# Optimization experiments

Measured on AMD Instinct MI355X. Metric: run time of the kernel, lower is better.

## Reference

```python
import jax, jax.numpy as jnp
import numpy as np

N, EM, EW, L, S = 20000, 100000, 25000, 128, 6


def _mlp(x, W1, b1, W2, b2, g, beta):
    # Linear -> ReLU -> Linear -> LayerNorm
    h = jax.nn.relu(x @ W1 + b1) @ W2 + b2
    mu = jnp.mean(h, axis=-1, keepdims=True)
    var = jnp.mean((h - mu) ** 2, axis=-1, keepdims=True)
    return g * (h - mu) * jax.lax.rsqrt(var + 1e-5) + beta


def _scatter_mean(attr, recv, n):
    s = jax.ops.segment_sum(attr, recv, num_segments=n)
    c = jax.ops.segment_sum(jnp.ones((attr.shape[0], 1), attr.dtype), recv, num_segments=n)
    return s / jnp.maximum(c, 1.0)


def setup_inputs() -> dict:
    key = jax.random.key(0)
    ks = jax.random.split(key, 16)

    def w(k, shape, fan_in):
        return (jax.random.normal(k, shape, jnp.float32) / np.sqrt(fan_in).astype(np.float32))

    inp = {
        'x': jax.random.normal(ks[0], (N, L), jnp.float32),
        'mesh_edge_attr': jax.random.normal(ks[1], (EM, L), jnp.float32),
        'world_edge_attr': jax.random.normal(ks[2], (EW, L), jnp.float32),
        'mesh_edge_index': jax.random.randint(ks[3], (2, EM), 0, N),
        'world_edge_index': jax.random.randint(ks[4], (2, EW), 0, N),
    }
    i = 5
    for pre in ('me', 'we', 'nd'):
        inp[pre + '_W1'] = w(ks[i], (S, 3 * L, L), 3 * L); i += 1
        inp[pre + '_b1'] = jnp.zeros((S, L), jnp.float32)
        inp[pre + '_W2'] = w(ks[i], (S, L, L), L); i += 1
        inp[pre + '_b2'] = jnp.zeros((S, L), jnp.float32)
        inp[pre + '_g'] = jnp.ones((S, L), jnp.float32)
        inp[pre + '_beta'] = jnp.zeros((S, L), jnp.float32)
    return inp


def reference(x, mesh_edge_attr, world_edge_attr, mesh_edge_index, world_edge_index,
              me_W1, me_b1, me_W2, me_b2, me_g, me_beta,
              we_W1, we_b1, we_W2, we_b2, we_g, we_beta,
              nd_W1, nd_b1, nd_W2, nd_b2, nd_g, nd_beta):
    ms, mr = mesh_edge_index[0], mesh_edge_index[1]
    ws, wr = world_edge_index[0], world_edge_index[1]
    n = x.shape[0]

    def step(carry, p):
        x, mea, wea = carry
        (mW1, mb1, mW2, mb2, mg, mbe,
         wW1, wb1, wW2, wb2, wg, wbe,
         nW1, nb1, nW2, nb2, ng, nbe) = p
        # EdgeModel: gather + concat + MLP, residual into edge attrs
        mea = mea + _mlp(jnp.concatenate([x[ms], x[mr], mea], axis=-1), mW1, mb1, mW2, mb2, mg, mbe)
        wea = wea + _mlp(jnp.concatenate([x[ws], x[wr], wea], axis=-1), wW1, wb1, wW2, wb2, wg, wbe)
        # NodeModel: scatter-mean over both edge sets + concat + MLP, residual
        agg = jnp.concatenate([x, _scatter_mean(mea, mr, n), _scatter_mean(wea, wr, n)], axis=-1)
        x = x + _mlp(agg, nW1, nb1, nW2, nb2, ng, nbe)
        return (x, mea, wea), None

    params = (me_W1, me_b1, me_W2, me_b2, me_g, me_beta,
              we_W1, we_b1, we_W2, we_b2, we_g, we_beta,
              nd_W1, nd_b1, nd_W2, nd_b2, nd_g, nd_beta)
    (x, mea, wea), _ = jax.lax.scan(step, (x, mesh_edge_attr, world_edge_attr), params)
    return x, mea, wea
```

## Files before the change

### kernel.cpp

```cpp
#include <hip/hip_runtime.h>

constexpr int LDIM  = 128;
constexpr int NNODE = 20000;
constexpr int EM_N  = 100000;
constexpr int EW_N  = 25000;
constexpr int NSTEP = 6;

typedef short bf16x8 __attribute__((ext_vector_type(8)));
typedef short bf16x4 __attribute__((ext_vector_type(4)));
typedef float f32x4  __attribute__((ext_vector_type(4)));

struct MlpParams {
  const float* x;
  const float* attrIn;
  float*       attrOut;
  const int*   src;
  const int*   dst;
  float*       sum1;
  float*       sum2;
  const float* inv1;
  const float* inv2;
  const short* W1H;
  const short* W2H;
  const float* b1;
  const float* b2;
  const float* gam;
  const float* bet;
  int nRows;
};

__device__ __forceinline__ short f2b(float f) {
  unsigned int u = __float_as_uint(f);
  u = (u + 0x7fffu + ((u >> 16) & 1u)) >> 16;
  return (short)u;
}
__device__ __forceinline__ float b2f(short s) {
  return __uint_as_float(((unsigned int)(unsigned short)s) << 16);
}
__device__ __forceinline__ bf16x4 cvt4(float4 a, float sc) {
  bf16x4 o;
  o[0] = f2b(a.x * sc); o[1] = f2b(a.y * sc);
  o[2] = f2b(a.z * sc); o[3] = f2b(a.w * sc);
  return o;
}

template<bool IS_EDGE>
__launch_bounds__(256, 3)
__global__ void mlp_kernel(MlpParams pmA, MlpParams pmB, int blocksA) {
  const bool isA = (int)blockIdx.x < blocksA;
  const MlpParams P = isA ? pmA : pmB;
  const int bid  = isA ? (int)blockIdx.x : (int)blockIdx.x - blocksA;
  const int row0 = bid * 128;

  __shared__ __align__(16) short Hbuf[128][136];
  __shared__ __align__(16) short Bhi[128][40];
  __shared__ float b1s[128], b2s[128], gs[128], bes[128];
  __shared__ int   idxa[128], idxb[128];
  __shared__ float inv1s[128], inv2s[128];
  __shared__ float sumL[2][128], sqL[2][128];
  __shared__ float muL[128], rsL[128];

  short (*Abuf)[40] = (short (*)[40])(&Hbuf[0][0]);

  const int t = threadIdx.x;

  if (t < 128) {
    b1s[t] = P.b1[t];
    gs[t]  = P.gam[t];
    if (IS_EDGE) {
      int r = row0 + t;
      idxa[t] = (r < P.nRows) ? P.src[r] : 0;
    } else {
      int r = min(row0 + t, P.nRows - 1);
      inv1s[t] = P.inv1[r];
    }
  } else {
    int t2 = t - 128;
    b2s[t2] = P.b2[t2];
    bes[t2] = P.bet[t2];
    if (IS_EDGE) {
      int r = row0 + t2;
      idxb[t2] = (r < P.nRows) ? P.dst[r] : 0;
    } else {
      int r = min(row0 + t2, P.nRows - 1);
      inv2s[t2] = P.inv2[r];
    }
  }
  __syncthreads();

  const int l   = t & 63;
  const int wid = t >> 6;
  const int wr  = wid >> 1, wcc = wid & 1;
  const int lr  = l & 15,  lg  = l >> 4;

  const int  srow  = t >> 1, sh = t & 1;
  const int  sgRow = row0 + srow;
  const bool sval  = sgRow < P.nRows;
  const int  sgC   = sval ? sgRow : 0;
  const float vmask = sval ? 1.f : 0.f;

  const float* base0; const float* base1; const float* base2;
  float sc1v = vmask, sc2v = vmask;
  if (IS_EDGE) {
    base0 = P.x + (size_t)idxa[srow] * LDIM + sh * 16;
    base1 = P.x + (size_t)idxb[srow] * LDIM + sh * 16;
    base2 = P.attrIn + (size_t)sgC * LDIM + sh * 16;
  } else {
    base0 = P.x    + (size_t)sgC * LDIM + sh * 16;
    base1 = P.sum1 + (size_t)sgC * LDIM + sh * 16;
    base2 = P.sum2 + (size_t)sgC * LDIM + sh * 16;
    sc1v = inv1s[srow] * vmask;
    sc2v = inv2s[srow] * vmask;
  }

  const int wrow = t >> 1, wsh = t & 1;
  const short* w1base = P.W1H + (size_t)wrow * 384 + wsh * 16;

  f32x4 acc[4][4];
#pragma unroll
  for (int i = 0; i < 4; ++i)
#pragma unroll
    for (int j = 0; j < 4; ++j) acc[i][j] = f32x4{0.f, 0.f, 0.f, 0.f};

  float4 pA0, pA1, pA2, pA3;
  bf16x8 pW0, pW1;
  {
    const float4* bp = (const float4*)base0;
    pA0 = bp[0]; pA1 = bp[1]; pA2 = bp[2]; pA3 = bp[3];
    pW0 = *(const bf16x8*)w1base;
    pW1 = *(const bf16x8*)(w1base + 8);
  }

#pragma unroll
  for (int kc = 0; kc < 12; ++kc) {
    const int seg = kc >> 2, part = kc & 3;
    if (kc > 0) __syncthreads();
    {
      const float scK = (seg == 0) ? vmask : (seg == 1) ? sc1v : sc2v;
      *(bf16x4*)&Abuf[srow][sh * 16 + 0]  = cvt4(pA0, scK);
      *(bf16x4*)&Abuf[srow][sh * 16 + 4]  = cvt4(pA1, scK);
      *(bf16x4*)&Abuf[srow][sh * 16 + 8]  = cvt4(pA2, scK);
      *(bf16x4*)&Abuf[srow][sh * 16 + 12] = cvt4(pA3, scK);
      *(bf16x8*)&Bhi[wrow][wsh * 16]     = pW0;
      *(bf16x8*)&Bhi[wrow][wsh * 16 + 8] = pW1;
      if constexpr (!IS_EDGE) {
        if (seg != 0 && sval) {
          float4 z = {0.f, 0.f, 0.f, 0.f};
          float4* zp = (float4*)((seg == 1 ? base1 : base2) + part * 32);
          zp[0] = z; zp[1] = z; zp[2] = z; zp[3] = z;
        }
      }
    }
    __syncthreads();
    if (kc < 11) {
      const int kn = kc + 1, segn = kn >> 2, partn = kn & 3;
      const float4* bp = (const float4*)((segn == 0 ? base0 : segn == 1 ? base1 : base2) + partn * 32);
      pA0 = bp[0]; pA1 = bp[1]; pA2 = bp[2]; pA3 = bp[3];
      pW0 = *(const bf16x8*)(w1base + kn * 32);
      pW1 = *(const bf16x8*)(w1base + kn * 32 + 8);
    }
    bf16x8 av[4], bh[4];
#pragma unroll
    for (int mi = 0; mi < 4; ++mi)
      av[mi] = *(const bf16x8*)&Abuf[wr * 64 + mi * 16 + lr][lg * 8];
#pragma unroll
    for (int ni = 0; ni < 4; ++ni)
      bh[ni] = *(const bf16x8*)&Bhi[wcc * 64 + ni * 16 + lr][lg * 8];
#pragma unroll
    for (int mi = 0; mi < 4; ++mi)
#pragma unroll
      for (int ni = 0; ni < 4; ++ni)
        acc[mi][ni] = __builtin_amdgcn_mfma_f32_16x16x32_bf16(av[mi], bh[ni], acc[mi][ni], 0, 0, 0);
  }

  __syncthreads();

#pragma unroll
  for (int rt = 0; rt < 4; ++rt)
#pragma unroll
    for (int ct = 0; ct < 4; ++ct) {
      const int cc = wcc * 64 + ct * 16 + lr;
      const float bb = b1s[cc];
#pragma unroll
      for (int q = 0; q < 4; ++q) {
        const int rr = wr * 64 + rt * 16 + lg * 4 + q;
        Hbuf[rr][cc] = f2b(fmaxf(acc[rt][ct][q] + bb, 0.f));
      }
    }

  f32x4 acc2[4][4];
#pragma unroll
  for (int i = 0; i < 4; ++i)
#pragma unroll
    for (int j = 0; j < 4; ++j) acc2[i][j] = f32x4{0.f, 0.f, 0.f, 0.f};

  const short* w2base = P.W2H + (size_t)wrow * 128 + wsh * 16;
  bf16x8 q0 = *(const bf16x8*)w2base;
  bf16x8 q1 = *(const bf16x8*)(w2base + 8);

#pragma unroll
  for (int kc = 0; kc < 4; ++kc) {
    __syncthreads();
    {
      *(bf16x8*)&Bhi[wrow][wsh * 16]     = q0;
      *(bf16x8*)&Bhi[wrow][wsh * 16 + 8] = q1;
    }
    __syncthreads();
    if (kc < 3) {
      q0 = *(const bf16x8*)(w2base + (kc + 1) * 32);
      q1 = *(const bf16x8*)(w2base + (kc + 1) * 32 + 8);
    }
    bf16x8 av2[4], bh2[4];
#pragma unroll
    for (int rt = 0; rt < 4; ++rt)
      av2[rt] = *(const bf16x8*)&Hbuf[wr * 64 + rt * 16 + lr][kc * 32 + lg * 8];
#pragma unroll
    for (int ct = 0; ct < 4; ++ct)
      bh2[ct] = *(const bf16x8*)&Bhi[wcc * 64 + ct * 16 + lr][lg * 8];
#pragma unroll
    for (int rt = 0; rt < 4; ++rt)
#pragma unroll
      for (int ct = 0; ct < 4; ++ct)
        acc2[rt][ct] = __builtin_amdgcn_mfma_f32_16x16x32_bf16(av2[rt], bh2[ct], acc2[rt][ct], 0, 0, 0);
  }

  float s1[4][4], s2[4][4];
#pragma unroll
  for (int rt = 0; rt < 4; ++rt)
#pragma unroll
    for (int q = 0; q < 4; ++q) { s1[rt][q] = 0.f; s2[rt][q] = 0.f; }
#pragma unroll
  for (int rt = 0; rt < 4; ++rt)
#pragma unroll
    for (int ct = 0; ct < 4; ++ct) {
      const float bb = b2s[wcc * 64 + ct * 16 + lr];
#pragma unroll
      for (int q = 0; q < 4; ++q) {
        float v = acc2[rt][ct][q] + bb;
        acc2[rt][ct][q] = v;
        s1[rt][q] += v;
        s2[rt][q] += v * v;
      }
    }
#pragma unroll
  for (int m = 1; m < 16; m <<= 1) {
#pragma unroll
    for (int rt = 0; rt < 4; ++rt)
#pragma unroll
      for (int q = 0; q < 4; ++q) {
        s1[rt][q] += __shfl_xor(s1[rt][q], m);
        s2[rt][q] += __shfl_xor(s2[rt][q], m);
      }
  }
  __syncthreads();
  {
    const int rt = lr >> 2, q = lr & 3;
    const int rr = wr * 64 + rt * 16 + lg * 4 + q;
    sumL[wcc][rr] = s1[rt][q];
    sqL[wcc][rr]  = s2[rt][q];
  }
  __syncthreads();
  if (t < 128) {
    const float tot = sumL[0][t] + sumL[1][t];
    const float tsq = sqL[0][t] + sqL[1][t];
    const float mu  = tot * (1.0f / 128.0f);
    const float var = tsq * (1.0f / 128.0f) - mu * mu;
    muL[t] = mu;
    rsL[t] = rsqrtf(var + 1e-5f);
  }
  __syncthreads();

#pragma unroll
  for (int rt = 0; rt < 4; ++rt) {
#pragma unroll
    for (int q = 0; q < 4; ++q) {
      const int rr = wr * 64 + rt * 16 + lg * 4 + q;
      const int grow = row0 + rr;
      if (grow < P.nRows) {
        const float mu = muL[rr], rs = rsL[rr];
        const float* rin = P.attrIn + (size_t)grow * LDIM;
        float* rout = P.attrOut + (size_t)grow * LDIM;
        float* ssum = nullptr;
        if (IS_EDGE) ssum = P.sum1 + (size_t)idxb[rr] * LDIM;
#pragma unroll
        for (int ct = 0; ct < 4; ++ct) {
          const int cc = wcc * 64 + ct * 16 + lr;
          const float o = gs[cc] * (acc2[rt][ct][q] - mu) * rs + bes[cc] + rin[cc];
          rout[cc] = o;
          if (IS_EDGE) atomicAdd(ssum + cc, o);
        }
      }
    }
  }
}

__global__ void prep_weights(const float* w1a, const float* w1b, const float* w1c,
                             const float* w2a, const float* w2b, const float* w2c,
                             short* w1h, short* w2h) {
  int i = blockIdx.x * 256 + threadIdx.x;
  constexpr int N1 = 18 * 128 * 384;
  constexpr int N2 = 18 * 128 * 128;
  if (i < N1) {
    int g = i / (128 * 384);
    int rem = i - g * (128 * 384);
    int n = rem / 384, k = rem - n * 384;
    int m = g / 6, s = g - m * 6;
    const float* src = (m == 0) ? w1a : (m == 1) ? w1b : w1c;
    w1h[i] = f2b(src[(size_t)s * (384 * 128) + (size_t)k * 128 + n]);
  } else if (i < N1 + N2) {
    int j = i - N1;
    int g = j / (128 * 128);
    int rem = j - g * (128 * 128);
    int n = rem / 128, k = rem - n * 128;
    int m = g / 6, s = g - m * 6;
    const float* src = (m == 0) ? w2a : (m == 1) ? w2b : w2c;
    w2h[j] = f2b(src[(size_t)s * (128 * 128) + (size_t)k * 128 + n]);
  }
}

__global__ void prep_deg(const int* mr, const int* wrcv, int* degm, int* degw) {
  int i = blockIdx.x * 256 + threadIdx.x;
  if (i < EM_N) atomicAdd(&degm[mr[i]], 1);
  else if (i < EM_N + EW_N) atomicAdd(&degw[wrcv[i - EM_N]], 1);
}

__global__ void prep_inv(const int* degm, const int* degw, float* invm, float* invw) {
  int i = blockIdx.x * 256 + threadIdx.x;
  if (i < NNODE) {
    invm[i] = 1.0f / fmaxf((float)degm[i], 1.0f);
    invw[i] = 1.0f / fmaxf((float)degw[i], 1.0f);
  }
}

extern "C" void kernel_launch(void* const* d_in, const int* in_sizes, int n_in,
                              void* d_out, int out_size, void* d_ws, size_t ws_size,
                              hipStream_t stream) {
  (void)in_sizes; (void)n_in; (void)out_size; (void)ws_size;
  const float* x_in   = (const float*)d_in[0];
  const float* mea_in = (const float*)d_in[1];
  const float* wea_in = (const float*)d_in[2];
  const int*   mei    = (const int*)d_in[3];
  const int*   wei    = (const int*)d_in[4];
  const float* W1s[3] = { (const float*)d_in[5],  (const float*)d_in[11], (const float*)d_in[17] };
  const float* B1s[3] = { (const float*)d_in[6],  (const float*)d_in[12], (const float*)d_in[18] };
  const float* W2s[3] = { (const float*)d_in[7],  (const float*)d_in[13], (const float*)d_in[19] };
  const float* B2s[3] = { (const float*)d_in[8],  (const float*)d_in[14], (const float*)d_in[20] };
  const float* Gs[3]  = { (const float*)d_in[9],  (const float*)d_in[15], (const float*)d_in[21] };
  const float* Be[3]  = { (const float*)d_in[10], (const float*)d_in[16], (const float*)d_in[22] };

  float* xo  = (float*)d_out;
  float* meo = xo  + (size_t)NNODE * LDIM;
  float* weo = meo + (size_t)EM_N * LDIM;

  float* msum = (float*)d_ws;
  float* wsum = msum + (size_t)NNODE * LDIM;
  int*   degm = (int*)(wsum + (size_t)NNODE * LDIM);
  int*   degw = degm + NNODE;
  float* invm = (float*)(degw + NNODE);
  float* invw = invm + NNODE;
  short* w1h  = (short*)(invw + NNODE);
  short* w2h  = w1h + (size_t)18 * 128 * 384;

  size_t zbytes = (size_t)2 * NNODE * LDIM * 4 + (size_t)2 * NNODE * 4;
  hipMemsetAsync(d_ws, 0, zbytes, stream);

  {
    int tot = 18 * 128 * 384 + 18 * 128 * 128;
    prep_weights<<<dim3((tot + 255) / 256), 256, 0, stream>>>(
        W1s[0], W1s[1], W1s[2], W2s[0], W2s[1], W2s[2], w1h, w2h);
  }
  prep_deg<<<dim3((EM_N + EW_N + 255) / 256), 256, 0, stream>>>(mei + EM_N, wei + EW_N, degm, degw);
  prep_inv<<<dim3((NNODE + 255) / 256), 256, 0, stream>>>(degm, degw, invm, invw);

  const int MB = (EM_N + 127) / 128;
  const int WB = (EW_N + 127) / 128;
  const int NB = (NNODE + 127) / 128;

  const float* xc = x_in;
  const float* mc = mea_in;
  const float* wc = wea_in;

  for (int s = 0; s < NSTEP; ++s) {
    MlpParams pm{}, pw{}, pn{};

    pm.x = xc; pm.attrIn = mc; pm.attrOut = meo;
    pm.src = mei; pm.dst = mei + EM_N;
    pm.sum1 = msum;
    pm.W1H = w1h + (size_t)(0 * 6 + s) * 128 * 384;
    pm.W2H = w2h + (size_t)(0 * 6 + s) * 128 * 128;
    pm.b1 = B1s[0] + s * LDIM; pm.b2 = B2s[0] + s * LDIM;
    pm.gam = Gs[0] + s * LDIM; pm.bet = Be[0] + s * LDIM;
    pm.nRows = EM_N;

    pw.x = xc; pw.attrIn = wc; pw.attrOut = weo;
    pw.src = wei; pw.dst = wei + EW_N;
    pw.sum1 = wsum;
    pw.W1H = w1h + (size_t)(1 * 6 + s) * 128 * 384;
    pw.W2H = w2h + (size_t)(1 * 6 + s) * 128 * 128;
    pw.b1 = B1s[1] + s * LDIM; pw.b2 = B2s[1] + s * LDIM;
    pw.gam = Gs[1] + s * LDIM; pw.bet = Be[1] + s * LDIM;
    pw.nRows = EW_N;

    mlp_kernel<true><<<dim3(MB + WB), 256, 0, stream>>>(pm, pw, MB);

    pn.x = xc; pn.attrIn = xc; pn.attrOut = xo;
    pn.sum1 = msum; pn.sum2 = wsum; pn.inv1 = invm; pn.inv2 = invw;
    pn.W1H = w1h + (size_t)(2 * 6 + s) * 128 * 384;
    pn.W2H = w2h + (size_t)(2 * 6 + s) * 128 * 128;
    pn.b1 = B1s[2] + s * LDIM; pn.b2 = B2s[2] + s * LDIM;
    pn.gam = Gs[2] + s * LDIM; pn.bet = Be[2] + s * LDIM;
    pn.nRows = NNODE;

    mlp_kernel<false><<<dim3(NB), 256, 0, stream>>>(pn, pn, NB);

    xc = xo; mc = meo; wc = weo;
  }
}
```

Measured before the change: 919.6 us.

## Double-buffer LDS staging in MLP GEMMs with single barrier per chunk

Converts both GEMM k-loops in the fused MLP kernel to double-buffered LDS staging, with two A buffers carved from Hbuf and two weight buffers. Global loads run two chunks ahead in register sets, and each iteration needs one barrier instead of two, using a custom waitcnt+s_barrier helper. This is meant to cut barrier stalls and overlap global loads with MFMA. In exchange it uses more registers and LDS, so launch bounds drop from 3 to 2 blocks per SM, which lowers occupancy.

New measurement: 1.047 ms. 1.14x slower.

```diff
diff --git a/kernel.cpp b/kernel.cpp
--- a/kernel.cpp
+++ b/kernel.cpp
@@ -44,8 +44,14 @@
   return o;
 }
 
+__device__ __forceinline__ void barrier_lds() {
+  asm volatile("s_waitcnt lgkmcnt(0)" ::: "memory");
+  __builtin_amdgcn_sched_barrier(0);
+  __builtin_amdgcn_s_barrier();
+}
+
 template<bool IS_EDGE>
-__launch_bounds__(256, 3)
+__launch_bounds__(256, 2)
 __global__ void mlp_kernel(MlpParams pmA, MlpParams pmB, int blocksA) {
   const bool isA = (int)blockIdx.x < blocksA;
   const MlpParams P = isA ? pmA : pmB;
@@ -53,14 +59,15 @@
   const int row0 = bid * 128;
 
   __shared__ __align__(16) short Hbuf[128][136];
-  __shared__ __align__(16) short Bhi[128][40];
+  __shared__ __align__(16) short Wst[2][128][40];
   __shared__ float b1s[128], b2s[128], gs[128], bes[128];
   __shared__ int   idxa[128], idxb[128];
   __shared__ float inv1s[128], inv2s[128];
   __shared__ float sumL[2][128], sqL[2][128];
   __shared__ float muL[128], rsL[128];
 
-  short (*Abuf)[40] = (short (*)[40])(&Hbuf[0][0]);
+  short (*Abuf0)[40] = (short (*)[40])(&Hbuf[0][0]);
+  short (*Abuf1)[40] = (short (*)[40])(&Hbuf[0][0] + 128 * 40);
 
   const int t = threadIdx.x;
 
@@ -122,58 +129,77 @@
 #pragma unroll
     for (int j = 0; j < 4; ++j) acc[i][j] = f32x4{0.f, 0.f, 0.f, 0.f};
 
-  float4 pA0, pA1, pA2, pA3;
-  bf16x8 pW0, pW1;
-  {
-    const float4* bp = (const float4*)base0;
-    pA0 = bp[0]; pA1 = bp[1]; pA2 = bp[2]; pA3 = bp[3];
-    pW0 = *(const bf16x8*)w1base;
-    pW1 = *(const bf16x8*)(w1base + 8);
-  }
-
-#pragma unroll
-  for (int kc = 0; kc < 12; ++kc) {
-    const int seg = kc >> 2, part = kc & 3;
-    if (kc > 0) __syncthreads();
-    {
-      const float scK = (seg == 0) ? vmask : (seg == 1) ? sc1v : sc2v;
-      *(bf16x4*)&Abuf[srow][sh * 16 + 0]  = cvt4(pA0, scK);
-      *(bf16x4*)&Abuf[srow][sh * 16 + 4]  = cvt4(pA1, scK);
-      *(bf16x4*)&Abuf[srow][sh * 16 + 8]  = cvt4(pA2, scK);
-      *(bf16x4*)&Abuf[srow][sh * 16 + 12] = cvt4(pA3, scK);
-      *(bf16x8*)&Bhi[wrow][wsh * 16]     = pW0;
-      *(bf16x8*)&Bhi[wrow][wsh * 16 + 8] = pW1;
-      if constexpr (!IS_EDGE) {
-        if (seg != 0 && sval) {
-          float4 z = {0.f, 0.f, 0.f, 0.f};
-          float4* zp = (float4*)((seg == 1 ? base1 : base2) + part * 32);
-          zp[0] = z; zp[1] = z; zp[2] = z; zp[3] = z;
-        }
-      }
-    }
-    __syncthreads();
-    if (kc < 11) {
-      const int kn = kc + 1, segn = kn >> 2, partn = kn & 3;
-      const float4* bp = (const float4*)((segn == 0 ? base0 : segn == 1 ? base1 : base2) + partn * 32);
-      pA0 = bp[0]; pA1 = bp[1]; pA2 = bp[2]; pA3 = bp[3];
-      pW0 = *(const bf16x8*)(w1base + kn * 32);
-      pW1 = *(const bf16x8*)(w1base + kn * 32 + 8);
-    }
+  float4 aE0, aE1, aE2, aE3, aO0, aO1, aO2, aO3;
+  bf16x8 wE0, wE1, wO0, wO1;
+
+  auto issueLoad = [&](int kn, float4& r0, float4& r1, float4& r2, float4& r3,
+                       bf16x8& w0, bf16x8& w1) {
+    const int seg = kn >> 2, part = kn & 3;
+    const float4* bp = (const float4*)((seg == 0 ? base0 : seg == 1 ? base1 : base2) + part * 32);
+    r0 = bp[0]; r1 = bp[1]; r2 = bp[2]; r3 = bp[3];
+    w0 = *(const bf16x8*)(w1base + kn * 32);
+    w1 = *(const bf16x8*)(w1base + kn * 32 + 8);
+  };
+
+  auto writeChunk = [&](short (*Ab)[40], short (*Wb)[40], int kw,
+                        float4 a0, float4 a1, float4 a2, float4 a3,
+                        bf16x8 w0, bf16x8 w1) {
+    const int seg = kw >> 2, part = kw & 3;
+    const float scK = (seg == 0) ? vmask : (seg == 1) ? sc1v : sc2v;
+    *(bf16x4*)&Ab[srow][sh * 16 + 0]  = cvt4(a0, scK);
+    *(bf16x4*)&Ab[srow][sh * 16 + 4]  = cvt4(a1, scK);
+    *(bf16x4*)&Ab[srow][sh * 16 + 8]  = cvt4(a2, scK);
+    *(bf16x4*)&Ab[srow][sh * 16 + 12] = cvt4(a3, scK);
+    *(bf16x8*)&Wb[wrow][wsh * 16]     = w0;
+    *(bf16x8*)&Wb[wrow][wsh * 16 + 8] = w1;
+    if constexpr (!IS_EDGE) {
+      if (seg != 0 && sval) {
+        float4 z = {0.f, 0.f, 0.f, 0.f};
+        float4* zp = (float4*)((seg == 1 ? base1 : base2) + part * 32);
+        zp[0] = z; zp[1] = z; zp[2] = z; zp[3] = z;
+      }
+    }
+  };
+
+  auto doMfma = [&](short (*Ab)[40], short (*Wb)[40]) {
     bf16x8 av[4], bh[4];
 #pragma unroll
     for (int mi = 0; mi < 4; ++mi)
-      av[mi] = *(const bf16x8*)&Abuf[wr * 64 + mi * 16 + lr][lg * 8];
+      av[mi] = *(const bf16x8*)&Ab[wr * 64 + mi * 16 + lr][lg * 8];
 #pragma unroll
     for (int ni = 0; ni < 4; ++ni)
-      bh[ni] = *(const bf16x8*)&Bhi[wcc * 64 + ni * 16 + lr][lg * 8];
+      bh[ni] = *(const bf16x8*)&Wb[wcc * 64 + ni * 16 + lr][lg * 8];
 #pragma unroll
     for (int mi = 0; mi < 4; ++mi)
 #pragma unroll
       for (int ni = 0; ni < 4; ++ni)
         acc[mi][ni] = __builtin_amdgcn_mfma_f32_16x16x32_bf16(av[mi], bh[ni], acc[mi][ni], 0, 0, 0);
-  }
-
-  __syncthreads();
+  };
+
+  issueLoad(0, aE0, aE1, aE2, aE3, wE0, wE1);
+  issueLoad(1, aO0, aO1, aO2, aO3, wO0, wO1);
+  writeChunk(Abuf0, Wst[0], 0, aE0, aE1, aE2, aE3, wE0, wE1);
+  barrier_lds();
+
+#pragma unroll
+  for (int kc = 0; kc < 12; ++kc) {
+    if ((kc & 1) == 0) {
+      if (kc + 1 < 12) writeChunk(Abuf1, Wst[1], kc + 1, aO0, aO1, aO2, aO3, wO0, wO1);
+      if (kc + 2 < 12) issueLoad(kc + 2, aE0, aE1, aE2, aE3, wE0, wE1);
+      doMfma(Abuf0, Wst[0]);
+    } else {
+      if (kc + 1 < 12) writeChunk(Abuf0, Wst[0], kc + 1, aE0, aE1, aE2, aE3, wE0, wE1);
+      if (kc + 2 < 12) issueLoad(kc + 2, aO0, aO1, aO2, aO3, wO0, wO1);
+      doMfma(Abuf1, Wst[1]);
+    }
+    barrier_lds();
+  }
+
+  const short* w2base = P.W2H + (size_t)wrow * 128 + wsh * 16;
+  bf16x8 vE0 = *(const bf16x8*)(w2base);
+  bf16x8 vE1 = *(const bf16x8*)(w2base + 8);
+  bf16x8 vO0 = *(const bf16x8*)(w2base + 32);
+  bf16x8 vO1 = *(const bf16x8*)(w2base + 40);
 
 #pragma unroll
   for (int rt = 0; rt < 4; ++rt)
@@ -187,6 +213,9 @@
         Hbuf[rr][cc] = f2b(fmaxf(acc[rt][ct][q] + bb, 0.f));
       }
     }
+  *(bf16x8*)&Wst[0][wrow][wsh * 16]     = vE0;
+  *(bf16x8*)&Wst[0][wrow][wsh * 16 + 8] = vE1;
+  barrier_lds();
 
   f32x4 acc2[4][4];
 #pragma unroll
@@ -194,34 +223,45 @@
 #pragma unroll
     for (int j = 0; j < 4; ++j) acc2[i][j] = f32x4{0.f, 0.f, 0.f, 0.f};
 
-  const short* w2base = P.W2H + (size_t)wrow * 128 + wsh * 16;
-  bf16x8 q0 = *(const bf16x8*)w2base;
-  bf16x8 q1 = *(const bf16x8*)(w2base + 8);
-
-#pragma unroll
-  for (int kc = 0; kc < 4; ++kc) {
-    __syncthreads();
-    {
-      *(bf16x8*)&Bhi[wrow][wsh * 16]     = q0;
-      *(bf16x8*)&Bhi[wrow][wsh * 16 + 8] = q1;
-    }
-    __syncthreads();
-    if (kc < 3) {
-      q0 = *(const bf16x8*)(w2base + (kc + 1) * 32);
-      q1 = *(const bf16x8*)(w2base + (kc + 1) * 32 + 8);
-    }
+  auto doMfma2 = [&](short (*Wb)[40], int kc) {
     bf16x8 av2[4], bh2[4];
 #pragma unroll
     for (int rt = 0; rt < 4; ++rt)
       av2[rt] = *(const bf16x8*)&Hbuf[wr * 64 + rt * 16 + lr][kc * 32 + lg * 8];
 #pragma unroll
     for (int ct = 0; ct < 4; ++ct)
-      bh2[ct] = *(const bf16x8*)&Bhi[wcc * 64 + ct * 16 + lr][lg * 8];
+      bh2[ct] = *(const bf16x8*)&Wb[wcc * 64 + ct * 16 + lr][lg * 8];
 #pragma unroll
     for (int rt = 0; rt < 4; ++rt)
 #pragma unroll
       for (int ct = 0; ct < 4; ++ct)
         acc2[rt][ct] = __builtin_amdgcn_mfma_f32_16x16x32_bf16(av2[rt], bh2[ct], acc2[rt][ct], 0, 0, 0);
+  };
+
+#pragma unroll
+  for (int kc = 0; kc < 4; ++kc) {
+    if ((kc & 1) == 0) {
+      if (kc + 1 < 4) {
+        *(bf16x8*)&Wst[1][wrow][wsh * 16]     = vO0;
+        *(bf16x8*)&Wst[1][wrow][wsh * 16 + 8] = vO1;
+      }
+      if (kc + 2 < 4) {
+        vE0 = *(const bf16x8*)(w2base + (kc + 2) * 32);
+        vE1 = *(const bf16x8*)(w2base + (kc + 2) * 32 + 8);
+      }
+      doMfma2(Wst[0], kc);
+    } else {
+      if (kc + 1 < 4) {
+        *(bf16x8*)&Wst[0][wrow][wsh * 16]     = vE0;
+        *(bf16x8*)&Wst[0][wrow][wsh * 16 + 8] = vE1;
+      }
+      if (kc + 2 < 4) {
+        vO0 = *(const bf16x8*)(w2base + (kc + 2) * 32);
+        vO1 = *(const bf16x8*)(w2base + (kc + 2) * 32 + 8);
+      }
+      doMfma2(Wst[1], kc);
+    }
+    barrier_lds();
   }
 
   float s1[4][4], s2[4][4];
```

## Restructure MLP kernel so each wave owns 16 rows with no block syncs

Applied to the files above, without the earlier changes.

Replaces the 128-row block tile, which staged A and W1/W2 through shared memory with block-wide barriers, with a per-wave 16-row tile. Each wave loads its A fragments straight from global memory into MFMA registers and reads weight fragments directly from global memory (L2-cached). It keeps only a small per-wave LDS buffer for the hidden activations and does the LayerNorm reduction within the wave using shuffles. Conversion to bf16 now uses the packed v_cvt_pk_bf16_f32 instruction, and blocks cover 64 rows each. This removes the __syncthreads and LDS round-trips, but weights are no longer reused across rows through shared memory, so global and L2 weight traffic rises, and the direct global fragment loads are less coalesced.

After: 1.374 ms. 49.4% more time.

```diff
diff --git a/kernel.cpp b/kernel.cpp
--- a/kernel.cpp
+++ b/kernel.cpp
@@ -7,7 +7,6 @@
 constexpr int NSTEP = 6;
 
 typedef short bf16x8 __attribute__((ext_vector_type(8)));
-typedef short bf16x4 __attribute__((ext_vector_type(4)));
 typedef float f32x4  __attribute__((ext_vector_type(4)));
 
 struct MlpParams {
@@ -34,261 +33,147 @@
   u = (u + 0x7fffu + ((u >> 16) & 1u)) >> 16;
   return (short)u;
 }
-__device__ __forceinline__ float b2f(short s) {
-  return __uint_as_float(((unsigned int)(unsigned short)s) << 16);
-}
-__device__ __forceinline__ bf16x4 cvt4(float4 a, float sc) {
-  bf16x4 o;
-  o[0] = f2b(a.x * sc); o[1] = f2b(a.y * sc);
-  o[2] = f2b(a.z * sc); o[3] = f2b(a.w * sc);
-  return o;
+
+__device__ __forceinline__ unsigned int cvtpk(float lo, float hi) {
+  unsigned int r;
+  asm("v_cvt_pk_bf16_f32 %0, %1, %2" : "=v"(r) : "v"(lo), "v"(hi));
+  return r;
+}
+__device__ __forceinline__ bf16x8 pack8(float4 a, float4 b) {
+  union { unsigned int u[4]; bf16x8 s; } x;
+  x.u[0] = cvtpk(a.x, a.y); x.u[1] = cvtpk(a.z, a.w);
+  x.u[2] = cvtpk(b.x, b.y); x.u[3] = cvtpk(b.z, b.w);
+  return x.s;
 }
 
 template<bool IS_EDGE>
 __launch_bounds__(256, 3)
 __global__ void mlp_kernel(MlpParams pmA, MlpParams pmB, int blocksA) {
+  __shared__ __align__(16) short HwAll[4][16][136];
+
+  const int t   = threadIdx.x;
+  const int wid = t >> 6, l = t & 63;
+  const int lr  = l & 15,  lg = l >> 4;
+  short (*Hw)[136] = HwAll[wid];
+
   const bool isA = (int)blockIdx.x < blocksA;
   const MlpParams P = isA ? pmA : pmB;
   const int bid  = isA ? (int)blockIdx.x : (int)blockIdx.x - blocksA;
-  const int row0 = bid * 128;
-
-  __shared__ __align__(16) short Hbuf[128][136];
-  __shared__ __align__(16) short Bhi[128][40];
-  __shared__ float b1s[128], b2s[128], gs[128], bes[128];
-  __shared__ int   idxa[128], idxb[128];
-  __shared__ float inv1s[128], inv2s[128];
-  __shared__ float sumL[2][128], sqL[2][128];
-  __shared__ float muL[128], rsL[128];
-
-  short (*Abuf)[40] = (short (*)[40])(&Hbuf[0][0]);
-
-  const int t = threadIdx.x;
-
-  if (t < 128) {
-    b1s[t] = P.b1[t];
-    gs[t]  = P.gam[t];
-    if (IS_EDGE) {
-      int r = row0 + t;
-      idxa[t] = (r < P.nRows) ? P.src[r] : 0;
-    } else {
-      int r = min(row0 + t, P.nRows - 1);
-      inv1s[t] = P.inv1[r];
-    }
+  const int r0   = bid * 64 + wid * 16;
+
+  const int  arow = min(r0 + lr, P.nRows - 1);
+  const bool aval = (r0 + lr) < P.nRows;
+
+  const float* base0; const float* base1; const float* base2;
+  float sc1 = 1.f, sc2 = 1.f;
+  if (IS_EDGE) {
+    base0 = P.x + (size_t)P.src[arow] * LDIM;
+    base1 = P.x + (size_t)P.dst[arow] * LDIM;
+    base2 = P.attrIn + (size_t)arow * LDIM;
   } else {
-    int t2 = t - 128;
-    b2s[t2] = P.b2[t2];
-    bes[t2] = P.bet[t2];
-    if (IS_EDGE) {
-      int r = row0 + t2;
-      idxb[t2] = (r < P.nRows) ? P.dst[r] : 0;
-    } else {
-      int r = min(row0 + t2, P.nRows - 1);
-      inv2s[t2] = P.inv2[r];
-    }
-  }
-  __syncthreads();
-
-  const int l   = t & 63;
-  const int wid = t >> 6;
-  const int wr  = wid >> 1, wcc = wid & 1;
-  const int lr  = l & 15,  lg  = l >> 4;
-
-  const int  srow  = t >> 1, sh = t & 1;
-  const int  sgRow = row0 + srow;
-  const bool sval  = sgRow < P.nRows;
-  const int  sgC   = sval ? sgRow : 0;
-  const float vmask = sval ? 1.f : 0.f;
-
-  const float* base0; const float* base1; const float* base2;
-  float sc1v = vmask, sc2v = vmask;
-  if (IS_EDGE) {
-    base0 = P.x + (size_t)idxa[srow] * LDIM + sh * 16;
-    base1 = P.x + (size_t)idxb[srow] * LDIM + sh * 16;
-    base2 = P.attrIn + (size_t)sgC * LDIM + sh * 16;
-  } else {
-    base0 = P.x    + (size_t)sgC * LDIM + sh * 16;
-    base1 = P.sum1 + (size_t)sgC * LDIM + sh * 16;
-    base2 = P.sum2 + (size_t)sgC * LDIM + sh * 16;
-    sc1v = inv1s[srow] * vmask;
-    sc2v = inv2s[srow] * vmask;
-  }
-
-  const int wrow = t >> 1, wsh = t & 1;
-  const short* w1base = P.W1H + (size_t)wrow * 384 + wsh * 16;
-
-  f32x4 acc[4][4];
-#pragma unroll
-  for (int i = 0; i < 4; ++i)
-#pragma unroll
-    for (int j = 0; j < 4; ++j) acc[i][j] = f32x4{0.f, 0.f, 0.f, 0.f};
-
-  float4 pA0, pA1, pA2, pA3;
-  bf16x8 pW0, pW1;
-  {
-    const float4* bp = (const float4*)base0;
-    pA0 = bp[0]; pA1 = bp[1]; pA2 = bp[2]; pA3 = bp[3];
-    pW0 = *(const bf16x8*)w1base;
-    pW1 = *(const bf16x8*)(w1base + 8);
-  }
+    base0 = P.x    + (size_t)arow * LDIM;
+    base1 = P.sum1 + (size_t)arow * LDIM;
+    base2 = P.sum2 + (size_t)arow * LDIM;
+    sc1 = P.inv1[arow];
+    sc2 = P.inv2[arow];
+  }
+
+  const short* w1p = P.W1H + (size_t)lr * 384 + lg * 8;
+  f32x4 acc[8];
+#pragma unroll
+  for (int i = 0; i < 8; ++i) acc[i] = f32x4{0.f, 0.f, 0.f, 0.f};
 
 #pragma unroll
   for (int kc = 0; kc < 12; ++kc) {
     const int seg = kc >> 2, part = kc & 3;
-    if (kc > 0) __syncthreads();
-    {
-      const float scK = (seg == 0) ? vmask : (seg == 1) ? sc1v : sc2v;
-      *(bf16x4*)&Abuf[srow][sh * 16 + 0]  = cvt4(pA0, scK);
-      *(bf16x4*)&Abuf[srow][sh * 16 + 4]  = cvt4(pA1, scK);
-      *(bf16x4*)&Abuf[srow][sh * 16 + 8]  = cvt4(pA2, scK);
-      *(bf16x4*)&Abuf[srow][sh * 16 + 12] = cvt4(pA3, scK);
-      *(bf16x8*)&Bhi[wrow][wsh * 16]     = pW0;
-      *(bf16x8*)&Bhi[wrow][wsh * 16 + 8] = pW1;
-      if constexpr (!IS_EDGE) {
-        if (seg != 0 && sval) {
+    const float* ab = (seg == 0 ? base0 : seg == 1 ? base1 : base2) + part * 32 + lg * 8;
+    float4 a0 = *(const float4*)ab;
+    float4 a1 = *(const float4*)(ab + 4);
+    if constexpr (!IS_EDGE) {
+      if (seg != 0) {
+        const float sc = (seg == 1) ? sc1 : sc2;
+        a0.x *= sc; a0.y *= sc; a0.z *= sc; a0.w *= sc;
+        a1.x *= sc; a1.y *= sc; a1.z *= sc; a1.w *= sc;
+        if (aval) {
           float4 z = {0.f, 0.f, 0.f, 0.f};
-          float4* zp = (float4*)((seg == 1 ? base1 : base2) + part * 32);
-          zp[0] = z; zp[1] = z; zp[2] = z; zp[3] = z;
+          ((float4*)ab)[0] = z; ((float4*)ab)[1] = z;
         }
       }
     }
-    __syncthreads();
-    if (kc < 11) {
-      const int kn = kc + 1, segn = kn >> 2, partn = kn & 3;
-      const float4* bp = (const float4*)((segn == 0 ? base0 : segn == 1 ? base1 : base2) + partn * 32);
-      pA0 = bp[0]; pA1 = bp[1]; pA2 = bp[2]; pA3 = bp[3];
-      pW0 = *(const bf16x8*)(w1base + kn * 32);
-      pW1 = *(const bf16x8*)(w1base + kn * 32 + 8);
-    }
-    bf16x8 av[4], bh[4];
-#pragma unroll
-    for (int mi = 0; mi < 4; ++mi)
-      av[mi] = *(const bf16x8*)&Abuf[wr * 64 + mi * 16 + lr][lg * 8];
-#pragma unroll
-    for (int ni = 0; ni < 4; ++ni)
-      bh[ni] = *(const bf16x8*)&Bhi[wcc * 64 + ni * 16 + lr][lg * 8];
-#pragma unroll
-    for (int mi = 0; mi < 4; ++mi)
-#pragma unroll
-      for (int ni = 0; ni < 4; ++ni)
-        acc[mi][ni] = __builtin_amdgcn_mfma_f32_16x16x32_bf16(av[mi], bh[ni], acc[mi][ni], 0, 0, 0);
-  }
-
-  __syncthreads();
-
-#pragma unroll
-  for (int rt = 0; rt < 4; ++rt)
-#pragma unroll
-    for (int ct = 0; ct < 4; ++ct) {
-      const int cc = wcc * 64 + ct * 16 + lr;
-      const float bb = b1s[cc];
-#pragma unroll
-      for (int q = 0; q < 4; ++q) {
-        const int rr = wr * 64 + rt * 16 + lg * 4 + q;
-        Hbuf[rr][cc] = f2b(fmaxf(acc[rt][ct][q] + bb, 0.f));
-      }
-    }
-
-  f32x4 acc2[4][4];
-#pragma unroll
-  for (int i = 0; i < 4; ++i)
-#pragma unroll
-    for (int j = 0; j < 4; ++j) acc2[i][j] = f32x4{0.f, 0.f, 0.f, 0.f};
-
-  const short* w2base = P.W2H + (size_t)wrow * 128 + wsh * 16;
-  bf16x8 q0 = *(const bf16x8*)w2base;
-  bf16x8 q1 = *(const bf16x8*)(w2base + 8);
+    const bf16x8 af = pack8(a0, a1);
+#pragma unroll
+    for (int ct = 0; ct < 8; ++ct) {
+      const bf16x8 bf = *(const bf16x8*)(w1p + (size_t)ct * (16 * 384) + kc * 32);
+      acc[ct] = __builtin_amdgcn_mfma_f32_16x16x32_bf16(af, bf, acc[ct], 0, 0, 0);
+    }
+  }
+
+#pragma unroll
+  for (int ct = 0; ct < 8; ++ct) {
+    const int cc = ct * 16 + lr;
+    const float bb = P.b1[cc];
+#pragma unroll
+    for (int q = 0; q < 4; ++q)
+      Hw[lg * 4 + q][cc] = f2b(fmaxf(acc[ct][q] + bb, 0.f));
+  }
+
+  const short* w2p = P.W2H + (size_t)lr * 128 + lg * 8;
+  f32x4 acc2[8];
+#pragma unroll
+  for (int i = 0; i < 8; ++i) acc2[i] = f32x4{0.f, 0.f, 0.f, 0.f};
 
 #pragma unroll
   for (int kc = 0; kc < 4; ++kc) {
-    __syncthreads();
-    {
-      *(bf16x8*)&Bhi[wrow][wsh * 16]     = q0;
-      *(bf16x8*)&Bhi[wrow][wsh * 16 + 8] = q1;
-    }
-    __syncthreads();
-    if (kc < 3) {
-      q0 = *(const bf16x8*)(w2base + (kc + 1) * 32);
-      q1 = *(const bf16x8*)(w2base + (kc + 1) * 32 + 8);
-    }
-    bf16x8 av2[4], bh2[4];
-#pragma unroll
-    for (int rt = 0; rt < 4; ++rt)
-      av2[rt] = *(const bf16x8*)&Hbuf[wr * 64 + rt * 16 + lr][kc * 32 + lg * 8];
-#pragma unroll
-    for (int ct = 0; ct < 4; ++ct)
-      bh2[ct] = *(const bf16x8*)&Bhi[wcc * 64 + ct * 16 + lr][lg * 8];
-#pragma unroll
-    for (int rt = 0; rt < 4; ++rt)
-#pragma unroll
-      for (int ct = 0; ct < 4; ++ct)
-        acc2[rt][ct] = __builtin_amdgcn_mfma_f32_16x16x32_bf16(av2[rt], bh2[ct], acc2[rt][ct], 0, 0, 0);
-  }
-
-  float s1[4][4], s2[4][4];
-#pragma unroll
-  for (int rt = 0; rt < 4; ++rt)
-#pragma unroll
-    for (int q = 0; q < 4; ++q) { s1[rt][q] = 0.f; s2[rt][q] = 0.f; }
-#pragma unroll
-  for (int rt = 0; rt < 4; ++rt)
-#pragma unroll
-    for (int ct = 0; ct < 4; ++ct) {
-      const float bb = b2s[wcc * 64 + ct * 16 + lr];
-#pragma unroll
-      for (int q = 0; q < 4; ++q) {
-        float v = acc2[rt][ct][q] + bb;
-        acc2[rt][ct][q] = v;
-        s1[rt][q] += v;
-        s2[rt][q] += v * v;
-      }
+    const bf16x8 hf = *(const bf16x8*)&Hw[lr][kc * 32 + lg * 8];
+#pragma unroll
+    for (int ct = 0; ct < 8; ++ct) {
+      const bf16x8 bf = *(const bf16x8*)(w2p + (size_t)ct * (16 * 128) + kc * 32);
+      acc2[ct] = __builtin_amdgcn_mfma_f32_16x16x32_bf16(hf, bf, acc2[ct], 0, 0, 0);
+    }
+  }
+
+  float bv[8], gv[8], bev[8];
+#pragma unroll
+  for (int ct = 0; ct < 8; ++ct) {
+    const int cc = ct * 16 + lr;
+    bv[ct] = P.b2[cc]; gv[ct] = P.gam[cc]; bev[ct] = P.bet[cc];
+  }
+  float s1a[4] = {0.f, 0.f, 0.f, 0.f};
+  float s2a[4] = {0.f, 0.f, 0.f, 0.f};
+#pragma unroll
+  for (int ct = 0; ct < 8; ++ct)
+#pragma unroll
+    for (int q = 0; q < 4; ++q) {
+      const float v = acc2[ct][q] + bv[ct];
+      acc2[ct][q] = v;
+      s1a[q] += v; s2a[q] += v * v;
     }
 #pragma unroll
   for (int m = 1; m < 16; m <<= 1) {
 #pragma unroll
-    for (int rt = 0; rt < 4; ++rt)
-#pragma unroll
-      for (int q = 0; q < 4; ++q) {
-        s1[rt][q] += __shfl_xor(s1[rt][q], m);
-        s2[rt][q] += __shfl_xor(s2[rt][q], m);
-      }
-  }
-  __syncthreads();
-  {
-    const int rt = lr >> 2, q = lr & 3;
-    const int rr = wr * 64 + rt * 16 + lg * 4 + q;
-    sumL[wcc][rr] = s1[rt][q];
-    sqL[wcc][rr]  = s2[rt][q];
-  }
-  __syncthreads();
-  if (t < 128) {
-    const float tot = sumL[0][t] + sumL[1][t];
-    const float tsq = sqL[0][t] + sqL[1][t];
-    const float mu  = tot * (1.0f / 128.0f);
-    const float var = tsq * (1.0f / 128.0f) - mu * mu;
-    muL[t] = mu;
-    rsL[t] = rsqrtf(var + 1e-5f);
-  }
-  __syncthreads();
-
-#pragma unroll
-  for (int rt = 0; rt < 4; ++rt) {
-#pragma unroll
     for (int q = 0; q < 4; ++q) {
-      const int rr = wr * 64 + rt * 16 + lg * 4 + q;
-      const int grow = row0 + rr;
-      if (grow < P.nRows) {
-        const float mu = muL[rr], rs = rsL[rr];
-        const float* rin = P.attrIn + (size_t)grow * LDIM;
-        float* rout = P.attrOut + (size_t)grow * LDIM;
-        float* ssum = nullptr;
-        if (IS_EDGE) ssum = P.sum1 + (size_t)idxb[rr] * LDIM;
-#pragma unroll
-        for (int ct = 0; ct < 4; ++ct) {
-          const int cc = wcc * 64 + ct * 16 + lr;
-          const float o = gs[cc] * (acc2[rt][ct][q] - mu) * rs + bes[cc] + rin[cc];
-          rout[cc] = o;
-          if (IS_EDGE) atomicAdd(ssum + cc, o);
-        }
+      s1a[q] += __shfl_xor(s1a[q], m);
+      s2a[q] += __shfl_xor(s2a[q], m);
+    }
+  }
+
+#pragma unroll
+  for (int q = 0; q < 4; ++q) {
+    const int grow = r0 + lg * 4 + q;
+    if (grow < P.nRows) {
+      const float mu  = s1a[q] * (1.0f / 128.0f);
+      const float var = s2a[q] * (1.0f / 128.0f) - mu * mu;
+      const float rs  = rsqrtf(var + 1e-5f);
+      const float* rin  = P.attrIn  + (size_t)grow * LDIM;
+      float*       rout = P.attrOut + (size_t)grow * LDIM;
+      float* ssum = nullptr;
+      if (IS_EDGE) ssum = P.sum1 + (size_t)P.dst[grow] * LDIM;
+#pragma unroll
+      for (int ct = 0; ct < 8; ++ct) {
+        const int cc = ct * 16 + lr;
+        const float o = gv[ct] * (acc2[ct][q] - mu) * rs + bev[ct] + rin[cc];
+        rout[cc] = o;
+        if (IS_EDGE) atomicAdd(ssum + cc, o);
       }
     }
   }
@@ -372,9 +257,9 @@
   prep_deg<<<dim3((EM_N + EW_N + 255) / 256), 256, 0, stream>>>(mei + EM_N, wei + EW_N, degm, degw);
   prep_inv<<<dim3((NNODE + 255) / 256), 256, 0, stream>>>(degm, degw, invm, invw);
 
-  const int MB = (EM_N + 127) / 128;
-  const int WB = (EW_N + 127) / 128;
-  const int NB = (NNODE + 127) / 128;
+  const int MB = (EM_N + 63) / 64;
+  const int WB = (EW_N + 63) / 64;
+  const int NB = (NNODE + 63) / 64;
 
   const float* xc = x_in;
   const float* mc = mea_in;
```

## Stage full 128-wide K chunks in LDS and use packed bf16 conversion

Applied to the files above, without the earlier changes.

Restructures both GEMM phases of the fused MLP kernel. The first GEMM now stages 128-wide K slices (three iterations instead of twelve 32-wide ones) for activations and W1 into full-width LDS tiles. W2 is loaded once into LDS before the second GEMM, which removes the per-chunk double barriers. Float-to-bf16 conversion uses the packed v_cvt_pk_bf16_f32 instruction, and the launch bound is lowered to 2 blocks per CU to fit the larger LDS footprint and register arrays. The aim is fewer barriers and cheaper conversion, at the cost of losing the register prefetch overlap and reducing occupancy.

Result: slower. 939.8 us (+2.2%).

```diff
diff --git a/kernel.cpp b/kernel.cpp
--- a/kernel.cpp
+++ b/kernel.cpp
@@ -7,7 +7,6 @@
 constexpr int NSTEP = 6;
 
 typedef short bf16x8 __attribute__((ext_vector_type(8)));
-typedef short bf16x4 __attribute__((ext_vector_type(4)));
 typedef float f32x4  __attribute__((ext_vector_type(4)));
 
 struct MlpParams {
@@ -34,18 +33,20 @@
   u = (u + 0x7fffu + ((u >> 16) & 1u)) >> 16;
   return (short)u;
 }
-__device__ __forceinline__ float b2f(short s) {
-  return __uint_as_float(((unsigned int)(unsigned short)s) << 16);
-}
-__device__ __forceinline__ bf16x4 cvt4(float4 a, float sc) {
-  bf16x4 o;
-  o[0] = f2b(a.x * sc); o[1] = f2b(a.y * sc);
-  o[2] = f2b(a.z * sc); o[3] = f2b(a.w * sc);
-  return o;
+__device__ __forceinline__ unsigned int cvtpk(float lo, float hi) {
+  unsigned int r;
+  asm("v_cvt_pk_bf16_f32 %0, %1, %2" : "=v"(r) : "v"(lo), "v"(hi));
+  return r;
+}
+__device__ __forceinline__ bf16x8 pack8(float4 a, float4 b) {
+  union { unsigned int u[4]; bf16x8 s; } x;
+  x.u[0] = cvtpk(a.x, a.y); x.u[1] = cvtpk(a.z, a.w);
+  x.u[2] = cvtpk(b.x, b.y); x.u[3] = cvtpk(b.z, b.w);
+  return x.s;
 }
 
 template<bool IS_EDGE>
-__launch_bounds__(256, 3)
+__launch_bounds__(256, 2)
 __global__ void mlp_kernel(MlpParams pmA, MlpParams pmB, int blocksA) {
   const bool isA = (int)blockIdx.x < blocksA;
   const MlpParams P = isA ? pmA : pmB;
@@ -53,14 +54,12 @@
   const int row0 = bid * 128;
 
   __shared__ __align__(16) short Hbuf[128][136];
-  __shared__ __align__(16) short Bhi[128][40];
+  __shared__ __align__(16) short Wst[128][136];
   __shared__ float b1s[128], b2s[128], gs[128], bes[128];
   __shared__ int   idxa[128], idxb[128];
   __shared__ float inv1s[128], inv2s[128];
   __shared__ float sumL[2][128], sqL[2][128];
   __shared__ float muL[128], rsL[128];
-
-  short (*Abuf)[40] = (short (*)[40])(&Hbuf[0][0]);
 
   const int t = threadIdx.x;
 
@@ -102,19 +101,19 @@
   const float* base0; const float* base1; const float* base2;
   float sc1v = vmask, sc2v = vmask;
   if (IS_EDGE) {
-    base0 = P.x + (size_t)idxa[srow] * LDIM + sh * 16;
-    base1 = P.x + (size_t)idxb[srow] * LDIM + sh * 16;
-    base2 = P.attrIn + (size_t)sgC * LDIM + sh * 16;
+    base0 = P.x + (size_t)idxa[srow] * LDIM + sh * 64;
+    base1 = P.x + (size_t)idxb[srow] * LDIM + sh * 64;
+    base2 = P.attrIn + (size_t)sgC * LDIM + sh * 64;
   } else {
-    base0 = P.x    + (size_t)sgC * LDIM + sh * 16;
-    base1 = P.sum1 + (size_t)sgC * LDIM + sh * 16;
-    base2 = P.sum2 + (size_t)sgC * LDIM + sh * 16;
+    base0 = P.x    + (size_t)sgC * LDIM + sh * 64;
+    base1 = P.sum1 + (size_t)sgC * LDIM + sh * 64;
+    base2 = P.sum2 + (size_t)sgC * LDIM + sh * 64;
     sc1v = inv1s[srow] * vmask;
     sc2v = inv2s[srow] * vmask;
   }
 
   const int wrow = t >> 1, wsh = t & 1;
-  const short* w1base = P.W1H + (size_t)wrow * 384 + wsh * 16;
+  const short* w1base = P.W1H + (size_t)wrow * 384 + wsh * 64;
 
   f32x4 acc[4][4];
 #pragma unroll
@@ -122,58 +121,63 @@
 #pragma unroll
     for (int j = 0; j < 4; ++j) acc[i][j] = f32x4{0.f, 0.f, 0.f, 0.f};
 
-  float4 pA0, pA1, pA2, pA3;
-  bf16x8 pW0, pW1;
-  {
-    const float4* bp = (const float4*)base0;
-    pA0 = bp[0]; pA1 = bp[1]; pA2 = bp[2]; pA3 = bp[3];
-    pW0 = *(const bf16x8*)w1base;
-    pW1 = *(const bf16x8*)(w1base + 8);
-  }
-
-#pragma unroll
-  for (int kc = 0; kc < 12; ++kc) {
-    const int seg = kc >> 2, part = kc & 3;
-    if (kc > 0) __syncthreads();
+#pragma unroll
+  for (int kc = 0; kc < 3; ++kc) {
     {
-      const float scK = (seg == 0) ? vmask : (seg == 1) ? sc1v : sc2v;
-      *(bf16x4*)&Abuf[srow][sh * 16 + 0]  = cvt4(pA0, scK);
-      *(bf16x4*)&Abuf[srow][sh * 16 + 4]  = cvt4(pA1, scK);
-      *(bf16x4*)&Abuf[srow][sh * 16 + 8]  = cvt4(pA2, scK);
-      *(bf16x4*)&Abuf[srow][sh * 16 + 12] = cvt4(pA3, scK);
-      *(bf16x8*)&Bhi[wrow][wsh * 16]     = pW0;
-      *(bf16x8*)&Bhi[wrow][wsh * 16 + 8] = pW1;
+      const float* abase = (kc == 0) ? base0 : (kc == 1) ? base1 : base2;
+      const float scK = (kc == 0) ? vmask : (kc == 1) ? sc1v : sc2v;
+      float4 av4[16];
+#pragma unroll
+      for (int j = 0; j < 16; ++j) av4[j] = ((const float4*)abase)[j];
+      if (scK != 1.0f) {
+#pragma unroll
+        for (int j = 0; j < 16; ++j) {
+          av4[j].x *= scK; av4[j].y *= scK; av4[j].z *= scK; av4[j].w *= scK;
+        }
+      }
       if constexpr (!IS_EDGE) {
-        if (seg != 0 && sval) {
+        if (kc != 0 && sval) {
           float4 z = {0.f, 0.f, 0.f, 0.f};
-          float4* zp = (float4*)((seg == 1 ? base1 : base2) + part * 32);
-          zp[0] = z; zp[1] = z; zp[2] = z; zp[3] = z;
+#pragma unroll
+          for (int j = 0; j < 16; ++j) ((float4*)abase)[j] = z;
         }
       }
+#pragma unroll
+      for (int j = 0; j < 8; ++j)
+        *(bf16x8*)&Hbuf[srow][sh * 64 + j * 8] = pack8(av4[2 * j], av4[2 * j + 1]);
+    }
+    {
+      const short* wsrc = w1base + kc * 128;
+      bf16x8 wv[8];
+#pragma unroll
+      for (int j = 0; j < 8; ++j) wv[j] = *(const bf16x8*)(wsrc + j * 8);
+#pragma unroll
+      for (int j = 0; j < 8; ++j)
+        *(bf16x8*)&Wst[wrow][wsh * 64 + j * 8] = wv[j];
     }
     __syncthreads();
-    if (kc < 11) {
-      const int kn = kc + 1, segn = kn >> 2, partn = kn & 3;
-      const float4* bp = (const float4*)((segn == 0 ? base0 : segn == 1 ? base1 : base2) + partn * 32);
-      pA0 = bp[0]; pA1 = bp[1]; pA2 = bp[2]; pA3 = bp[3];
-      pW0 = *(const bf16x8*)(w1base + kn * 32);
-      pW1 = *(const bf16x8*)(w1base + kn * 32 + 8);
-    }
-    bf16x8 av[4], bh[4];
-#pragma unroll
-    for (int mi = 0; mi < 4; ++mi)
-      av[mi] = *(const bf16x8*)&Abuf[wr * 64 + mi * 16 + lr][lg * 8];
-#pragma unroll
-    for (int ni = 0; ni < 4; ++ni)
-      bh[ni] = *(const bf16x8*)&Bhi[wcc * 64 + ni * 16 + lr][lg * 8];
-#pragma unroll
-    for (int mi = 0; mi < 4; ++mi)
+#pragma unroll
+    for (int kk = 0; kk < 4; ++kk) {
+      bf16x8 av[4], bh[4];
+#pragma unroll
+      for (int mi = 0; mi < 4; ++mi)
+        av[mi] = *(const bf16x8*)&Hbuf[wr * 64 + mi * 16 + lr][kk * 32 + lg * 8];
 #pragma unroll
       for (int ni = 0; ni < 4; ++ni)
-        acc[mi][ni] = __builtin_amdgcn_mfma_f32_16x16x32_bf16(av[mi], bh[ni], acc[mi][ni], 0, 0, 0);
-  }
-
-  __syncthreads();
+        bh[ni] = *(const bf16x8*)&Wst[wcc * 64 + ni * 16 + lr][kk * 32 + lg * 8];
+#pragma unroll
+      for (int mi = 0; mi < 4; ++mi)
+#pragma unroll
+        for (int ni = 0; ni < 4; ++ni)
+          acc[mi][ni] = __builtin_amdgcn_mfma_f32_16x16x32_bf16(av[mi], bh[ni], acc[mi][ni], 0, 0, 0);
+    }
+    __syncthreads();
+  }
+
+  const short* w2base = P.W2H + (size_t)wrow * 128 + wsh * 64;
+  bf16x8 w2v[8];
+#pragma unroll
+  for (int j = 0; j < 8; ++j) w2v[j] = *(const bf16x8*)(w2base + j * 8);
 
 #pragma unroll
   for (int rt = 0; rt < 4; ++rt)
@@ -187,6 +191,10 @@
         Hbuf[rr][cc] = f2b(fmaxf(acc[rt][ct][q] + bb, 0.f));
       }
     }
+#pragma unroll
+  for (int j = 0; j < 8; ++j)
+    *(bf16x8*)&Wst[wrow][wsh * 64 + j * 8] = w2v[j];
+  __syncthreads();
 
   f32x4 acc2[4][4];
 #pragma unroll
@@ -194,29 +202,15 @@
 #pragma unroll
     for (int j = 0; j < 4; ++j) acc2[i][j] = f32x4{0.f, 0.f, 0.f, 0.f};
 
-  const short* w2base = P.W2H + (size_t)wrow * 128 + wsh * 16;
-  bf16x8 q0 = *(const bf16x8*)w2base;
-  bf16x8 q1 = *(const bf16x8*)(w2base + 8);
-
-#pragma unroll
-  for (int kc = 0; kc < 4; ++kc) {
-    __syncthreads();
-    {
-      *(bf16x8*)&Bhi[wrow][wsh * 16]     = q0;
-      *(bf16x8*)&Bhi[wrow][wsh * 16 + 8] = q1;
-    }
-    __syncthreads();
-    if (kc < 3) {
-      q0 = *(const bf16x8*)(w2base + (kc + 1) * 32);
-      q1 = *(const bf16x8*)(w2base + (kc + 1) * 32 + 8);
-    }
+#pragma unroll
+  for (int kk = 0; kk < 4; ++kk) {
     bf16x8 av2[4], bh2[4];
 #pragma unroll
     for (int rt = 0; rt < 4; ++rt)
-      av2[rt] = *(const bf16x8*)&Hbuf[wr * 64 + rt * 16 + lr][kc * 32 + lg * 8];
+      av2[rt] = *(const bf16x8*)&Hbuf[wr * 64 + rt * 16 + lr][kk * 32 + lg * 8];
 #pragma unroll
     for (int ct = 0; ct < 4; ++ct)
-      bh2[ct] = *(const bf16x8*)&Bhi[wcc * 64 + ct * 16 + lr][lg * 8];
+      bh2[ct] = *(const bf16x8*)&Wst[wcc * 64 + ct * 16 + lr][kk * 32 + lg * 8];
 #pragma unroll
     for (int rt = 0; rt < 4; ++rt)
 #pragma unroll
```
